# Kernel tuning notes

Measured on AMD Instinct MI355X. Metric: run time of the kernel, lower is better.

## Reference

```python
import jax, jax.numpy as jnp
import numpy as np

B, C, N = 8, 256, 2048
H = max(1, C // 8)  # hidden = in_channels // 8 = 32


def setup_inputs() -> dict:
    key = jax.random.key(0)
    ks = jax.random.split(key, 7)
    s = 0.05
    return {
        "x": jax.random.normal(ks[0], (B, C, N), dtype=jnp.float32),
        "wq": jax.random.normal(ks[1], (H, C), dtype=jnp.float32) * s,
        "bq": jax.random.normal(ks[2], (H,), dtype=jnp.float32) * s,
        "wk": jax.random.normal(ks[3], (H, C), dtype=jnp.float32) * s,
        "bk": jax.random.normal(ks[4], (H,), dtype=jnp.float32) * s,
        "wv": jax.random.normal(ks[5], (C, C), dtype=jnp.float32) * s,
        "bv": jax.random.normal(ks[6], (C,), dtype=jnp.float32) * s,
    }


def reference(x, wq, bq, wk, bk, wv, bv):
    # 1x1 Conv1d == per-position linear: weight [out, in]
    q = jnp.einsum('bcn,hc->bnh', x, wq) + bq                  # [B, N, H] (already permuted)
    k = jnp.einsum('bcn,hc->bhn', x, wk) + bk[None, :, None]   # [B, H, N]
    v = jnp.einsum('bcn,dc->bdn', x, wv) + bv[None, :, None]   # [B, C, N]
    energy = jnp.einsum('bnh,bhm->bnm', q, k)                  # [B, N, N] (no scaling, as in source)
    weights = jax.nn.softmax(energy, axis=-1)                  # softmax over last dim
    # out = bmm(value, weights^T): out[b,c,i] = sum_j v[b,c,j] * weights[b,i,j]
    out = jnp.einsum('bcj,bij->bci', v, weights)               # [B, C, N]
    return out + x
```

## Files before the change

kernel.cpp:

```cpp
#include <hip/hip_runtime.h>
#include <hip/hip_bf16.h>
#include <cstdint>
#include <cstddef>

#define B_ 8
#define C_ 256
#define N_ 2048
#define H_ 32
#define VP_ 2064
#define NT_ (N_ / 64)

typedef __bf16 bf8 __attribute__((ext_vector_type(8)));
typedef __bf16 bf4 __attribute__((ext_vector_type(4)));
typedef float f4 __attribute__((ext_vector_type(4)));

__device__ inline void gload_lds16(const void* g, void* l) {
  __builtin_amdgcn_global_load_lds(
      (const __attribute__((address_space(1))) unsigned int*)g,
      (__attribute__((address_space(3))) unsigned int*)l, 16, 0, 0);
}

__global__ __launch_bounds__(256) void pack_kernel(
    const float* __restrict__ wq, const float* __restrict__ wk,
    const float* __restrict__ wv, const float* __restrict__ bq,
    const float* __restrict__ bk, const float* __restrict__ bv,
    __hip_bfloat16* __restrict__ wpk, float* __restrict__ bpk) {
  const float L2E = 1.44269504088896f;
  int r = blockIdx.x, c = threadIdx.x;
  float v;
  if (r < 256)      v = wv[r * 256 + c];
  else if (r < 288) v = wq[(r - 256) * 256 + c] * L2E;
  else              v = wk[(r - 288) * 256 + c];
  wpk[r * 256 + c] = __float2bfloat16(v);
  if (c == 0) bpk[r] = (r < 256) ? bv[r] : (r < 288 ? bq[r - 256] * L2E : bk[r - 288]);
}

__global__ __launch_bounds__(256) void proj_kernel(
    const float* __restrict__ x, const __hip_bfloat16* __restrict__ wpk,
    const float* __restrict__ bpk, __hip_bfloat16* __restrict__ vbf,
    __hip_bfloat16* __restrict__ qkb) {
  __shared__ __attribute__((aligned(16))) __hip_bfloat16 As[2][320 * 32];
  __shared__ __attribute__((aligned(16))) float xS[3][32 * 32];
  int tid = threadIdx.x, wv = tid >> 6, lane = tid & 63;
  int b = blockIdx.y;
  int n0 = blockIdx.x * 32;
  int fcol = lane & 15, hi4 = lane >> 4;
  int grow = lane >> 2, gc = (lane & 3) * 8;
  int xrow = wv * 8 + (lane >> 3), xcq = (lane & 7) * 4;
  const float* xb = x + (size_t)b * C_ * N_;

#pragma unroll
  for (int g = 0; g < 5; ++g)
    gload_lds16(wpk + (size_t)(wv * 80 + g * 16 + grow) * 256 + gc,
                &As[0][(wv * 80 + g * 16) * 32]);
  gload_lds16(xb + (size_t)xrow * N_ + n0 + xcq, &xS[0][wv * 8 * 32]);
  gload_lds16(xb + (size_t)(32 + xrow) * N_ + n0 + xcq, &xS[1][wv * 8 * 32]);

  f4 acc[5][2] = {};
  for (int t = 0; t < 8; ++t) {
    int buf = t & 1;
    if (t < 7)
      asm volatile("s_waitcnt vmcnt(1)" ::: "memory");
    else
      asm volatile("s_waitcnt vmcnt(0)" ::: "memory");
    __builtin_amdgcn_s_barrier();
    __builtin_amdgcn_sched_barrier(0);
    if (t < 7) {
      int k1 = (t + 1) * 32;
#pragma unroll
      for (int g = 0; g < 5; ++g)
        gload_lds16(wpk + (size_t)(wv * 80 + g * 16 + grow) * 256 + k1 + gc,
                    &As[buf ^ 1][(wv * 80 + g * 16) * 32]);
    }
    if (t < 6) {
      int k2 = (t + 2) * 32;
      gload_lds16(xb + (size_t)(k2 + xrow) * N_ + n0 + xcq,
                  &xS[(t + 2) % 3][wv * 8 * 32]);
    }
    const float* xt = &xS[t % 3][0];
    bf8 bfr[2];
#pragma unroll
    for (int j = 0; j < 2; ++j)
#pragma unroll
      for (int e = 0; e < 8; ++e)
        bfr[j][e] = (__bf16)xt[(hi4 * 8 + e) * 32 + j * 16 + fcol];
#pragma unroll
    for (int s = 0; s < 5; ++s) {
      bf8 af = *(const bf8*)&As[buf][(wv * 80 + s * 16 + fcol) * 32 + hi4 * 8];
      acc[s][0] = __builtin_amdgcn_mfma_f32_16x16x32_bf16(af, bfr[0], acc[s][0], 0, 0, 0);
      acc[s][1] = __builtin_amdgcn_mfma_f32_16x16x32_bf16(af, bfr[1], acc[s][1], 0, 0, 0);
    }
  }
  int rq = hi4 * 4;
#pragma unroll
  for (int s = 0; s < 5; ++s)
#pragma unroll
    for (int r = 0; r < 4; ++r) {
      int m = wv * 80 + s * 16 + rq + r;
      float bias = bpk[m];
#pragma unroll
      for (int j = 0; j < 2; ++j) {
        int n = n0 + j * 16 + fcol;
        float val = acc[s][j][r] + bias;
        if (m < 256)
          vbf[((size_t)b * C_ + m) * VP_ + n] = __float2bfloat16(val);
        else
          qkb[((size_t)b * N_ + n) * 64 + (m - 256)] = __float2bfloat16(val);
      }
    }
}

#define MFMA16(A, B, C) __builtin_amdgcn_mfma_f32_16x16x32_bf16(A, B, C, 0, 0, 0)

#define ATTN_BODY(T, BUF, KC0, KC1, KN0, KN1, VA, VB, VC, VD)                  \
  {                                                                            \
    bf8 pf00 = *(const bf8*)&pS[BUF][ 0 + li][ 0 + lg8];                       \
    bf8 pf10 = *(const bf8*)&pS[BUF][16 + li][ 0 + lg8];                       \
    bf8 pf20 = *(const bf8*)&pS[BUF][32 + li][ 0 + lg8];                       \
    bf8 pf30 = *(const bf8*)&pS[BUF][48 + li][ 0 + lg8];                       \
    bf8 pf01 = *(const bf8*)&pS[BUF][ 0 + li][32 + lg8];                       \
    bf8 pf11 = *(const bf8*)&pS[BUF][16 + li][32 + lg8];                       \
    bf8 pf21 = *(const bf8*)&pS[BUF][32 + li][32 + lg8];                       \
    bf8 pf31 = *(const bf8*)&pS[BUF][48 + li][32 + lg8];                       \
    f4 s00 = {}, s01 = {}, s10 = {}, s11 = {};                                 \
    if ((T) + 1 < NT_) {                                                       \
      s00 = MFMA16(KC0, qf0, s00);                                             \
      s01 = MFMA16(KC0, qf1, s01);                                             \
      s10 = MFMA16(KC1, qf0, s10);                                             \
      s11 = MFMA16(KC1, qf1, s11);                                             \
    }                                                                          \
    {                                                                          \
      int tn_ = (T) + 2 < NT_ ? (T) + 2 : NT_ - 1;                             \
      const __hip_bfloat16* kpn_ = kp + (size_t)tn_ * 64 * 64;                 \
      KN0 = *(const bf8*)kpn_;                                                 \
      KN1 = *(const bf8*)(kpn_ + 16 * 64);                                     \
    }                                                                          \
    __builtin_amdgcn_s_setprio(1);                                             \
    acc[0][0] = MFMA16(VA, pf00, acc[0][0]);                                   \
    acc[0][1] = MFMA16(VA, pf10, acc[0][1]);                                   \
    acc[0][2] = MFMA16(VA, pf20, acc[0][2]);                                   \
    acc[0][3] = MFMA16(VA, pf30, acc[0][3]);                                   \
    acc[1][0] = MFMA16(VC, pf00, acc[1][0]);                                   \
    acc[1][1] = MFMA16(VC, pf10, acc[1][1]);                                   \
    acc[1][2] = MFMA16(VC, pf20, acc[1][2]);                                   \
    acc[1][3] = MFMA16(VC, pf30, acc[1][3]);                                   \
    acc[0][0] = MFMA16(VB, pf01, acc[0][0]);                                   \
    acc[0][1] = MFMA16(VB, pf11, acc[0][1]);                                   \
    acc[0][2] = MFMA16(VB, pf21, acc[0][2]);                                   \
    acc[0][3] = MFMA16(VB, pf31, acc[0][3]);                                   \
    acc[1][0] = MFMA16(VD, pf01, acc[1][0]);                                   \
    acc[1][1] = MFMA16(VD, pf11, acc[1][1]);                                   \
    acc[1][2] = MFMA16(VD, pf21, acc[1][2]);                                   \
    acc[1][3] = MFMA16(VD, pf31, acc[1][3]);                                   \
    __builtin_amdgcn_s_setprio(0);                                             \
    {                                                                          \
      int tn_ = (T) + 2 < NT_ ? (T) + 2 : NT_ - 1;                             \
      const __hip_bfloat16* vpn_ = vR + tn_ * 64;                              \
      VA = *(const bf8*)vpn_;                                                  \
      VB = *(const bf8*)(vpn_ + 32);                                           \
      VC = *(const bf8*)(vpn_ + 16 * VP_);                                     \
      VD = *(const bf8*)(vpn_ + 16 * VP_ + 32);                                \
    }                                                                          \
    if ((T) + 1 < NT_) {                                                       \
      _Pragma("unroll")                                                        \
      for (int m = 0; m < 4; ++m) {                                            \
        s00[m] = __builtin_amdgcn_exp2f(s00[m]);                               \
        s01[m] = __builtin_amdgcn_exp2f(s01[m]);                               \
        s10[m] = __builtin_amdgcn_exp2f(s10[m]);                               \
        s11[m] = __builtin_amdgcn_exp2f(s11[m]);                               \
      }                                                                        \
      _Pragma("unroll")                                                        \
      for (int m = 0; m < 4; ++m) {                                            \
        lp0 += s00[m] + s10[m];                                                \
        lp1 += s01[m] + s11[m];                                                \
      }                                                                        \
      {                                                                        \
        bf4 t0, t1, t2, t3;                                                    \
        _Pragma("unroll")                                                      \
        for (int m = 0; m < 4; ++m) {                                          \
          t0[m] = (__bf16)s00[m]; t1[m] = (__bf16)s01[m];                      \
          t2[m] = (__bf16)s10[m]; t3[m] = (__bf16)s11[m];                      \
        }                                                                      \
        *(bf4*)&pS[(BUF) ^ 1][ws_i * 32 +  0 + li][ws_j * 32 +  0 + lg4] = t0; \
        *(bf4*)&pS[(BUF) ^ 1][ws_i * 32 + 16 + li][ws_j * 32 +  0 + lg4] = t1; \
        *(bf4*)&pS[(BUF) ^ 1][ws_i * 32 +  0 + li][ws_j * 32 + 16 + lg4] = t2; \
        *(bf4*)&pS[(BUF) ^ 1][ws_i * 32 + 16 + li][ws_j * 32 + 16 + lg4] = t3; \
      }                                                                        \
      asm volatile("s_waitcnt lgkmcnt(0)" ::: "memory");                       \
      __builtin_amdgcn_sched_barrier(0);                                       \
      __builtin_amdgcn_s_barrier();                                            \
      __builtin_amdgcn_sched_barrier(0);                                       \
    }                                                                          \
  }

__global__ __launch_bounds__(256, 2) void fused_attn(
    const __hip_bfloat16* __restrict__ qk,
    const __hip_bfloat16* __restrict__ vbf,
    const float* __restrict__ x, float* __restrict__ out) {
  __shared__ __attribute__((aligned(16))) __hip_bfloat16 pS[2][64][88];
  __shared__ float lSp[2][64];
  int tid = threadIdx.x;
  int wv = tid >> 6, lane = tid & 63;
  int li = lane & 15, lg = lane >> 4;
  int lg8 = lg * 8, lg4 = lg * 4;
  int ws_i = wv >> 1, ws_j = wv & 1;
  int blk = blockIdx.x;
  int b = blk & 7;
  int rest = blk >> 3;
  int c0 = (rest & 1) * 128;
  int i0 = (rest >> 1) * 64;

  const __hip_bfloat16* qkB = qk + (size_t)b * N_ * 64;
  bf8 qf0 = *(const bf8*)&qkB[(size_t)(i0 + ws_i * 32 +  0 + li) * 64 + lg8];
  bf8 qf1 = *(const bf8*)&qkB[(size_t)(i0 + ws_i * 32 + 16 + li) * 64 + lg8];
  const __hip_bfloat16* kp = qkB + (size_t)(ws_j * 32 + li) * 64 + 32 + lg8;
  const __hip_bfloat16* vR =
      vbf + ((size_t)b * C_ + c0 + wv * 32 + li) * VP_ + lg8;

  bf8 k00 = *(const bf8*)kp;
  bf8 k01 = *(const bf8*)(kp + 16 * 64);
  bf8 kO0 = *(const bf8*)(kp + 64 * 64);
  bf8 kO1 = *(const bf8*)(kp + 64 * 64 + 16 * 64);
  bf8 kE0, kE1;
  bf8 vEA = *(const bf8*)vR;
  bf8 vEB = *(const bf8*)(vR + 32);
  bf8 vEC = *(const bf8*)(vR + 16 * VP_);
  bf8 vED = *(const bf8*)(vR + 16 * VP_ + 32);
  bf8 vOA = *(const bf8*)(vR + 64);
  bf8 vOB = *(const bf8*)(vR + 64 + 32);
  bf8 vOC = *(const bf8*)(vR + 16 * VP_ + 64);
  bf8 vOD = *(const bf8*)(vR + 16 * VP_ + 64 + 32);

  f4 acc[2][4] = {};
  float lp0 = 0.f, lp1 = 0.f;

  {
    f4 s00 = {}, s01 = {}, s10 = {}, s11 = {};
    s00 = MFMA16(k00, qf0, s00);
    s01 = MFMA16(k00, qf1, s01);
    s10 = MFMA16(k01, qf0, s10);
    s11 = MFMA16(k01, qf1, s11);
#pragma unroll
    for (int m = 0; m < 4; ++m) {
      s00[m] = __builtin_amdgcn_exp2f(s00[m]);
      s01[m] = __builtin_amdgcn_exp2f(s01[m]);
      s10[m] = __builtin_amdgcn_exp2f(s10[m]);
      s11[m] = __builtin_amdgcn_exp2f(s11[m]);
    }
#pragma unroll
    for (int m = 0; m < 4; ++m) {
      lp0 += s00[m] + s10[m];
      lp1 += s01[m] + s11[m];
    }
    bf4 t0, t1, t2, t3;
#pragma unroll
    for (int m = 0; m < 4; ++m) {
      t0[m] = (__bf16)s00[m]; t1[m] = (__bf16)s01[m];
      t2[m] = (__bf16)s10[m]; t3[m] = (__bf16)s11[m];
    }
    *(bf4*)&pS[0][ws_i * 32 +  0 + li][ws_j * 32 +  0 + lg4] = t0;
    *(bf4*)&pS[0][ws_i * 32 + 16 + li][ws_j * 32 +  0 + lg4] = t1;
    *(bf4*)&pS[0][ws_i * 32 +  0 + li][ws_j * 32 + 16 + lg4] = t2;
    *(bf4*)&pS[0][ws_i * 32 + 16 + li][ws_j * 32 + 16 + lg4] = t3;
    asm volatile("s_waitcnt lgkmcnt(0)" ::: "memory");
    __builtin_amdgcn_sched_barrier(0);
    __builtin_amdgcn_s_barrier();
    __builtin_amdgcn_sched_barrier(0);
  }

  for (int tt = 0; tt < NT_; tt += 2) {
    ATTN_BODY(tt,     0, kO0, kO1, kE0, kE1, vEA, vEB, vEC, vED)
    ATTN_BODY(tt + 1, 1, kE0, kE1, kO0, kO1, vOA, vOB, vOC, vOD)
  }
#undef ATTN_BODY

  lp0 += __shfl_xor(lp0, 16); lp0 += __shfl_xor(lp0, 32);
  lp1 += __shfl_xor(lp1, 16); lp1 += __shfl_xor(lp1, 32);
  if (lane < 16)      lSp[ws_j][ws_i * 32 + lane] = lp0;
  else if (lane < 32) lSp[ws_j][ws_i * 32 + 16 + (lane & 15)] = lp1;
  __syncthreads();
  float linv0 = 1.0f / (lSp[0][ 0 + li] + lSp[1][ 0 + li]);
  float linv1 = 1.0f / (lSp[0][16 + li] + lSp[1][16 + li]);
  float linv2 = 1.0f / (lSp[0][32 + li] + lSp[1][32 + li]);
  float linv3 = 1.0f / (lSp[0][48 + li] + lSp[1][48 + li]);

  const float* xr = x + (size_t)b * C_ * N_;
  float* op = out + (size_t)b * C_ * N_;
#pragma unroll
  for (int cs = 0; cs < 2; ++cs)
#pragma unroll
    for (int m = 0; m < 4; ++m) {
      int c = c0 + wv * 32 + cs * 16 + lg4 + m;
      size_t base = (size_t)c * N_ + i0;
      op[base +  0 + li] = acc[cs][0][m] * linv0 + xr[base +  0 + li];
      op[base + 16 + li] = acc[cs][1][m] * linv1 + xr[base + 16 + li];
      op[base + 32 + li] = acc[cs][2][m] * linv2 + xr[base + 32 + li];
      op[base + 48 + li] = acc[cs][3][m] * linv3 + xr[base + 48 + li];
    }
}

extern "C" void kernel_launch(void* const* d_in, const int* in_sizes, int n_in,
                              void* d_out, int out_size, void* d_ws, size_t ws_size,
                              hipStream_t stream) {
  const float* x  = (const float*)d_in[0];
  const float* wq = (const float*)d_in[1];
  const float* bq = (const float*)d_in[2];
  const float* wk = (const float*)d_in[3];
  const float* bk = (const float*)d_in[4];
  const float* wv = (const float*)d_in[5];
  const float* bv = (const float*)d_in[6];
  float* out = (float*)d_out;

  char* ws = (char*)d_ws;
  __hip_bfloat16* qkb = (__hip_bfloat16*)ws;
  __hip_bfloat16* vbf = (__hip_bfloat16*)(ws + (2u << 20));
  __hip_bfloat16* wpk = (__hip_bfloat16*)(ws + 10551296u);
  float*          bpk = (float*)(ws + 10551296u + 163840u);

  pack_kernel<<<dim3(320), 256, 0, stream>>>(wq, wk, wv, bq, bk, bv, wpk, bpk);
  proj_kernel<<<dim3(N_ / 32, B_), 256, 0, stream>>>(x, wpk, bpk, vbf, qkb);
  fused_attn<<<dim3(512), 256, 0, stream>>>(qkb, vbf, x, out);
}
```

Baseline: 127.5 us.

## Halve attention query tile to 32 rows and deepen projection load pipeline

The fused attention kernel now gives each block 32 query rows instead of 64, launching 1024 blocks with a 4-blocks-per-SM launch bound. Each wave computes one 16-key slice of scores rather than a 2x2 split, and the row sums are reduced across four waves. The intent is more blocks and occupancy to hide latency, at the cost of streaming V and K twice as often per output. The projection kernel also moves from double to triple buffering of weights and quad buffering of x, with adjusted vmcnt waits to keep more loads in flight.

New measurement: 147.2 us. +15.5%, slower.

```diff
diff --git a/kernel.cpp b/kernel.cpp
--- a/kernel.cpp
+++ b/kernel.cpp
@@ -39,8 +39,8 @@
     const float* __restrict__ x, const __hip_bfloat16* __restrict__ wpk,
     const float* __restrict__ bpk, __hip_bfloat16* __restrict__ vbf,
     __hip_bfloat16* __restrict__ qkb) {
-  __shared__ __attribute__((aligned(16))) __hip_bfloat16 As[2][320 * 32];
-  __shared__ __attribute__((aligned(16))) float xS[3][32 * 32];
+  __shared__ __attribute__((aligned(16))) __hip_bfloat16 As[3][320 * 32];
+  __shared__ __attribute__((aligned(16))) float xS[4][32 * 32];
   int tid = threadIdx.x, wv = tid >> 6, lane = tid & 63;
   int b = blockIdx.y;
   int n0 = blockIdx.x * 32;
@@ -49,35 +49,32 @@
   int xrow = wv * 8 + (lane >> 3), xcq = (lane & 7) * 4;
   const float* xb = x + (size_t)b * C_ * N_;
 
-#pragma unroll
-  for (int g = 0; g < 5; ++g)
-    gload_lds16(wpk + (size_t)(wv * 80 + g * 16 + grow) * 256 + gc,
-                &As[0][(wv * 80 + g * 16) * 32]);
-  gload_lds16(xb + (size_t)xrow * N_ + n0 + xcq, &xS[0][wv * 8 * 32]);
-  gload_lds16(xb + (size_t)(32 + xrow) * N_ + n0 + xcq, &xS[1][wv * 8 * 32]);
+#define STAGE_W(T)                                                            \
+  _Pragma("unroll")                                                           \
+  for (int g = 0; g < 5; ++g)                                                 \
+    gload_lds16(wpk + (size_t)(wv * 80 + g * 16 + grow) * 256 + (T) * 32 + gc,\
+                &As[(T) % 3][(wv * 80 + g * 16) * 32]);
+#define STAGE_X(T)                                                            \
+  gload_lds16(xb + (size_t)((T) * 32 + xrow) * N_ + n0 + xcq,                 \
+              &xS[(T) % 4][wv * 8 * 32]);
+
+  STAGE_X(0)
+  STAGE_W(0)
+  STAGE_X(1)
+  STAGE_W(1)
+  STAGE_X(2)
 
   f4 acc[5][2] = {};
+#pragma unroll
   for (int t = 0; t < 8; ++t) {
-    int buf = t & 1;
-    if (t < 7)
-      asm volatile("s_waitcnt vmcnt(1)" ::: "memory");
-    else
-      asm volatile("s_waitcnt vmcnt(0)" ::: "memory");
+    if (t < 6)      asm volatile("s_waitcnt vmcnt(7)" ::: "memory");
+    else if (t == 6) asm volatile("s_waitcnt vmcnt(6)" ::: "memory");
+    else            asm volatile("s_waitcnt vmcnt(0)" ::: "memory");
     __builtin_amdgcn_s_barrier();
     __builtin_amdgcn_sched_barrier(0);
-    if (t < 7) {
-      int k1 = (t + 1) * 32;
-#pragma unroll
-      for (int g = 0; g < 5; ++g)
-        gload_lds16(wpk + (size_t)(wv * 80 + g * 16 + grow) * 256 + k1 + gc,
-                    &As[buf ^ 1][(wv * 80 + g * 16) * 32]);
-    }
-    if (t < 6) {
-      int k2 = (t + 2) * 32;
-      gload_lds16(xb + (size_t)(k2 + xrow) * N_ + n0 + xcq,
-                  &xS[(t + 2) % 3][wv * 8 * 32]);
-    }
-    const float* xt = &xS[t % 3][0];
+    if (t + 2 <= 7) { STAGE_W(t + 2) }
+    if (t + 3 <= 7) { STAGE_X(t + 3) }
+    const float* xt = &xS[t % 4][0];
     bf8 bfr[2];
 #pragma unroll
     for (int j = 0; j < 2; ++j)
@@ -86,11 +83,13 @@
         bfr[j][e] = (__bf16)xt[(hi4 * 8 + e) * 32 + j * 16 + fcol];
 #pragma unroll
     for (int s = 0; s < 5; ++s) {
-      bf8 af = *(const bf8*)&As[buf][(wv * 80 + s * 16 + fcol) * 32 + hi4 * 8];
+      bf8 af = *(const bf8*)&As[t % 3][(wv * 80 + s * 16 + fcol) * 32 + hi4 * 8];
       acc[s][0] = __builtin_amdgcn_mfma_f32_16x16x32_bf16(af, bfr[0], acc[s][0], 0, 0, 0);
       acc[s][1] = __builtin_amdgcn_mfma_f32_16x16x32_bf16(af, bfr[1], acc[s][1], 0, 0, 0);
     }
   }
+#undef STAGE_W
+#undef STAGE_X
   int rq = hi4 * 4;
 #pragma unroll
   for (int s = 0; s < 5; ++s)
@@ -112,46 +111,30 @@
 
 #define MFMA16(A, B, C) __builtin_amdgcn_mfma_f32_16x16x32_bf16(A, B, C, 0, 0, 0)
 
-#define ATTN_BODY(T, BUF, KC0, KC1, KN0, KN1, VA, VB, VC, VD)                  \
+#define ATTN_BODY(T, BUF, KC, KN, VA, VB, VC, VD)                              \
   {                                                                            \
     bf8 pf00 = *(const bf8*)&pS[BUF][ 0 + li][ 0 + lg8];                       \
     bf8 pf10 = *(const bf8*)&pS[BUF][16 + li][ 0 + lg8];                       \
-    bf8 pf20 = *(const bf8*)&pS[BUF][32 + li][ 0 + lg8];                       \
-    bf8 pf30 = *(const bf8*)&pS[BUF][48 + li][ 0 + lg8];                       \
     bf8 pf01 = *(const bf8*)&pS[BUF][ 0 + li][32 + lg8];                       \
     bf8 pf11 = *(const bf8*)&pS[BUF][16 + li][32 + lg8];                       \
-    bf8 pf21 = *(const bf8*)&pS[BUF][32 + li][32 + lg8];                       \
-    bf8 pf31 = *(const bf8*)&pS[BUF][48 + li][32 + lg8];                       \
-    f4 s00 = {}, s01 = {}, s10 = {}, s11 = {};                                 \
+    f4 s0 = {}, s1 = {};                                                       \
     if ((T) + 1 < NT_) {                                                       \
-      s00 = MFMA16(KC0, qf0, s00);                                             \
-      s01 = MFMA16(KC0, qf1, s01);                                             \
-      s10 = MFMA16(KC1, qf0, s10);                                             \
-      s11 = MFMA16(KC1, qf1, s11);                                             \
+      s0 = MFMA16(KC, qf0, s0);                                                \
+      s1 = MFMA16(KC, qf1, s1);                                                \
     }                                                                          \
     {                                                                          \
       int tn_ = (T) + 2 < NT_ ? (T) + 2 : NT_ - 1;                             \
-      const __hip_bfloat16* kpn_ = kp + (size_t)tn_ * 64 * 64;                 \
-      KN0 = *(const bf8*)kpn_;                                                 \
-      KN1 = *(const bf8*)(kpn_ + 16 * 64);                                     \
+      KN = *(const bf8*)(kp + (size_t)tn_ * 64 * 64);                          \
     }                                                                          \
     __builtin_amdgcn_s_setprio(1);                                             \
     acc[0][0] = MFMA16(VA, pf00, acc[0][0]);                                   \
     acc[0][1] = MFMA16(VA, pf10, acc[0][1]);                                   \
-    acc[0][2] = MFMA16(VA, pf20, acc[0][2]);                                   \
-    acc[0][3] = MFMA16(VA, pf30, acc[0][3]);                                   \
     acc[1][0] = MFMA16(VC, pf00, acc[1][0]);                                   \
     acc[1][1] = MFMA16(VC, pf10, acc[1][1]);                                   \
-    acc[1][2] = MFMA16(VC, pf20, acc[1][2]);                                   \
-    acc[1][3] = MFMA16(VC, pf30, acc[1][3]);                                   \
     acc[0][0] = MFMA16(VB, pf01, acc[0][0]);                                   \
     acc[0][1] = MFMA16(VB, pf11, acc[0][1]);                                   \
-    acc[0][2] = MFMA16(VB, pf21, acc[0][2]);                                   \
-    acc[0][3] = MFMA16(VB, pf31, acc[0][3]);                                   \
     acc[1][0] = MFMA16(VD, pf01, acc[1][0]);                                   \
     acc[1][1] = MFMA16(VD, pf11, acc[1][1]);                                   \
-    acc[1][2] = MFMA16(VD, pf21, acc[1][2]);                                   \
-    acc[1][3] = MFMA16(VD, pf31, acc[1][3]);                                   \
     __builtin_amdgcn_s_setprio(0);                                             \
     {                                                                          \
       int tn_ = (T) + 2 < NT_ ? (T) + 2 : NT_ - 1;                             \
@@ -164,28 +147,16 @@
     if ((T) + 1 < NT_) {                                                       \
       _Pragma("unroll")                                                        \
       for (int m = 0; m < 4; ++m) {                                            \
-        s00[m] = __builtin_amdgcn_exp2f(s00[m]);                               \
-        s01[m] = __builtin_amdgcn_exp2f(s01[m]);                               \
-        s10[m] = __builtin_amdgcn_exp2f(s10[m]);                               \
-        s11[m] = __builtin_amdgcn_exp2f(s11[m]);                               \
+        s0[m] = __builtin_amdgcn_exp2f(s0[m]);                                 \
+        s1[m] = __builtin_amdgcn_exp2f(s1[m]);                                 \
       }                                                                        \
+      lp0 += s0[0] + s0[1] + s0[2] + s0[3];                                    \
+      lp1 += s1[0] + s1[1] + s1[2] + s1[3];                                    \
+      bf4 t0, t1;                                                              \
       _Pragma("unroll")                                                        \
-      for (int m = 0; m < 4; ++m) {                                            \
-        lp0 += s00[m] + s10[m];                                                \
-        lp1 += s01[m] + s11[m];                                                \
-      }                                                                        \
-      {                                                                        \
-        bf4 t0, t1, t2, t3;                                                    \
-        _Pragma("unroll")                                                      \
-        for (int m = 0; m < 4; ++m) {                                          \
-          t0[m] = (__bf16)s00[m]; t1[m] = (__bf16)s01[m];                      \
-          t2[m] = (__bf16)s10[m]; t3[m] = (__bf16)s11[m];                      \
-        }                                                                      \
-        *(bf4*)&pS[(BUF) ^ 1][ws_i * 32 +  0 + li][ws_j * 32 +  0 + lg4] = t0; \
-        *(bf4*)&pS[(BUF) ^ 1][ws_i * 32 + 16 + li][ws_j * 32 +  0 + lg4] = t1; \
-        *(bf4*)&pS[(BUF) ^ 1][ws_i * 32 +  0 + li][ws_j * 32 + 16 + lg4] = t2; \
-        *(bf4*)&pS[(BUF) ^ 1][ws_i * 32 + 16 + li][ws_j * 32 + 16 + lg4] = t3; \
-      }                                                                        \
+      for (int m = 0; m < 4; ++m) { t0[m] = (__bf16)s0[m]; t1[m] = (__bf16)s1[m]; } \
+      *(bf4*)&pS[(BUF) ^ 1][ 0 + li][wv * 16 + lg4] = t0;                      \
+      *(bf4*)&pS[(BUF) ^ 1][16 + li][wv * 16 + lg4] = t1;                      \
       asm volatile("s_waitcnt lgkmcnt(0)" ::: "memory");                       \
       __builtin_amdgcn_sched_barrier(0);                                       \
       __builtin_amdgcn_s_barrier();                                            \
@@ -193,35 +164,32 @@
     }                                                                          \
   }
 
-__global__ __launch_bounds__(256, 2) void fused_attn(
+__global__ __launch_bounds__(256, 4) void fused_attn(
     const __hip_bfloat16* __restrict__ qk,
     const __hip_bfloat16* __restrict__ vbf,
     const float* __restrict__ x, float* __restrict__ out) {
-  __shared__ __attribute__((aligned(16))) __hip_bfloat16 pS[2][64][88];
-  __shared__ float lSp[2][64];
+  __shared__ __attribute__((aligned(16))) __hip_bfloat16 pS[2][32][72];
+  __shared__ float lSp[4][32];
   int tid = threadIdx.x;
   int wv = tid >> 6, lane = tid & 63;
   int li = lane & 15, lg = lane >> 4;
   int lg8 = lg * 8, lg4 = lg * 4;
-  int ws_i = wv >> 1, ws_j = wv & 1;
   int blk = blockIdx.x;
   int b = blk & 7;
   int rest = blk >> 3;
   int c0 = (rest & 1) * 128;
-  int i0 = (rest >> 1) * 64;
+  int i0 = (rest >> 1) * 32;
 
   const __hip_bfloat16* qkB = qk + (size_t)b * N_ * 64;
-  bf8 qf0 = *(const bf8*)&qkB[(size_t)(i0 + ws_i * 32 +  0 + li) * 64 + lg8];
-  bf8 qf1 = *(const bf8*)&qkB[(size_t)(i0 + ws_i * 32 + 16 + li) * 64 + lg8];
-  const __hip_bfloat16* kp = qkB + (size_t)(ws_j * 32 + li) * 64 + 32 + lg8;
+  bf8 qf0 = *(const bf8*)&qkB[(size_t)(i0 +  0 + li) * 64 + lg8];
+  bf8 qf1 = *(const bf8*)&qkB[(size_t)(i0 + 16 + li) * 64 + lg8];
+  const __hip_bfloat16* kp = qkB + (size_t)(wv * 16 + li) * 64 + 32 + lg8;
   const __hip_bfloat16* vR =
       vbf + ((size_t)b * C_ + c0 + wv * 32 + li) * VP_ + lg8;
 
   bf8 k00 = *(const bf8*)kp;
-  bf8 k01 = *(const bf8*)(kp + 16 * 64);
-  bf8 kO0 = *(const bf8*)(kp + 64 * 64);
-  bf8 kO1 = *(const bf8*)(kp + 64 * 64 + 16 * 64);
-  bf8 kE0, kE1;
+  bf8 kO = *(const bf8*)(kp + 64 * 64);
+  bf8 kE;
   bf8 vEA = *(const bf8*)vR;
   bf8 vEB = *(const bf8*)(vR + 32);
   bf8 vEC = *(const bf8*)(vR + 16 * VP_);
@@ -231,37 +199,25 @@
   bf8 vOC = *(const bf8*)(vR + 16 * VP_ + 64);
   bf8 vOD = *(const bf8*)(vR + 16 * VP_ + 64 + 32);
 
-  f4 acc[2][4] = {};
+  f4 acc[2][2] = {};
   float lp0 = 0.f, lp1 = 0.f;
 
   {
-    f4 s00 = {}, s01 = {}, s10 = {}, s11 = {};
-    s00 = MFMA16(k00, qf0, s00);
-    s01 = MFMA16(k00, qf1, s01);
-    s10 = MFMA16(k01, qf0, s10);
-    s11 = MFMA16(k01, qf1, s11);
+    f4 s0 = {}, s1 = {};
+    s0 = MFMA16(k00, qf0, s0);
+    s1 = MFMA16(k00, qf1, s1);
 #pragma unroll
     for (int m = 0; m < 4; ++m) {
-      s00[m] = __builtin_amdgcn_exp2f(s00[m]);
-      s01[m] = __builtin_amdgcn_exp2f(s01[m]);
-      s10[m] = __builtin_amdgcn_exp2f(s10[m]);
-      s11[m] = __builtin_amdgcn_exp2f(s11[m]);
-    }
-#pragma unroll
-    for (int m = 0; m < 4; ++m) {
-      lp0 += s00[m] + s10[m];
-      lp1 += s01[m] + s11[m];
-    }
-    bf4 t0, t1, t2, t3;
-#pragma unroll
-    for (int m = 0; m < 4; ++m) {
-      t0[m] = (__bf16)s00[m]; t1[m] = (__bf16)s01[m];
-      t2[m] = (__bf16)s10[m]; t3[m] = (__bf16)s11[m];
-    }
-    *(bf4*)&pS[0][ws_i * 32 +  0 + li][ws_j * 32 +  0 + lg4] = t0;
-    *(bf4*)&pS[0][ws_i * 32 + 16 + li][ws_j * 32 +  0 + lg4] = t1;
-    *(bf4*)&pS[0][ws_i * 32 +  0 + li][ws_j * 32 + 16 + lg4] = t2;
-    *(bf4*)&pS[0][ws_i * 32 + 16 + li][ws_j * 32 + 16 + lg4] = t3;
+      s0[m] = __builtin_amdgcn_exp2f(s0[m]);
+      s1[m] = __builtin_amdgcn_exp2f(s1[m]);
+    }
+    lp0 += s0[0] + s0[1] + s0[2] + s0[3];
+    lp1 += s1[0] + s1[1] + s1[2] + s1[3];
+    bf4 t0, t1;
+#pragma unroll
+    for (int m = 0; m < 4; ++m) { t0[m] = (__bf16)s0[m]; t1[m] = (__bf16)s1[m]; }
+    *(bf4*)&pS[0][ 0 + li][wv * 16 + lg4] = t0;
+    *(bf4*)&pS[0][16 + li][wv * 16 + lg4] = t1;
     asm volatile("s_waitcnt lgkmcnt(0)" ::: "memory");
     __builtin_amdgcn_sched_barrier(0);
     __builtin_amdgcn_s_barrier();
@@ -269,20 +225,18 @@
   }
 
   for (int tt = 0; tt < NT_; tt += 2) {
-    ATTN_BODY(tt,     0, kO0, kO1, kE0, kE1, vEA, vEB, vEC, vED)
-    ATTN_BODY(tt + 1, 1, kE0, kE1, kO0, kO1, vOA, vOB, vOC, vOD)
+    ATTN_BODY(tt,     0, kO, kE, vEA, vEB, vEC, vED)
+    ATTN_BODY(tt + 1, 1, kE, kO, vOA, vOB, vOC, vOD)
   }
 #undef ATTN_BODY
 
   lp0 += __shfl_xor(lp0, 16); lp0 += __shfl_xor(lp0, 32);
   lp1 += __shfl_xor(lp1, 16); lp1 += __shfl_xor(lp1, 32);
-  if (lane < 16)      lSp[ws_j][ws_i * 32 + lane] = lp0;
-  else if (lane < 32) lSp[ws_j][ws_i * 32 + 16 + (lane & 15)] = lp1;
+  if (lane < 16) { lSp[wv][lane] = lp0; lSp[wv][16 + lane] = lp1; }
   __syncthreads();
-  float linv0 = 1.0f / (lSp[0][ 0 + li] + lSp[1][ 0 + li]);
-  float linv1 = 1.0f / (lSp[0][16 + li] + lSp[1][16 + li]);
-  float linv2 = 1.0f / (lSp[0][32 + li] + lSp[1][32 + li]);
-  float linv3 = 1.0f / (lSp[0][48 + li] + lSp[1][48 + li]);
+  float linv0 = 1.0f / (lSp[0][li] + lSp[1][li] + lSp[2][li] + lSp[3][li]);
+  float linv1 = 1.0f / (lSp[0][16 + li] + lSp[1][16 + li] +
+                        lSp[2][16 + li] + lSp[3][16 + li]);
 
   const float* xr = x + (size_t)b * C_ * N_;
   float* op = out + (size_t)b * C_ * N_;
@@ -294,8 +248,6 @@
       size_t base = (size_t)c * N_ + i0;
       op[base +  0 + li] = acc[cs][0][m] * linv0 + xr[base +  0 + li];
       op[base + 16 + li] = acc[cs][1][m] * linv1 + xr[base + 16 + li];
-      op[base + 32 + li] = acc[cs][2][m] * linv2 + xr[base + 32 + li];
-      op[base + 48 + li] = acc[cs][3][m] * linv3 + xr[base + 48 + li];
     }
 }
 
@@ -319,5 +271,5 @@
 
   pack_kernel<<<dim3(320), 256, 0, stream>>>(wq, wk, wv, bq, bk, bv, wpk, bpk);
   proj_kernel<<<dim3(N_ / 32, B_), 256, 0, stream>>>(x, wpk, bpk, vbf, qkb);
-  fused_attn<<<dim3(512), 256, 0, stream>>>(qkb, vbf, x, out);
-}
+  fused_attn<<<dim3(1024), 256, 0, stream>>>(qkb, vbf, x, out);
+}
```
